# Optimization experiments

Measured on AMD Instinct MI355X. Metric: run time of the kernel, lower is better.

The kernel has to match this reference:

```python
import jax, jax.numpy as jnp
from jax import lax
import numpy as np

DIM = 192
WS = 8
HEADS = 6
HD = DIM // HEADS
SCALE = HD ** -0.5
EPS = 1e-6


def setup_inputs() -> dict:
    key = jax.random.key(0)
    ks = jax.random.split(key, 12)
    d = DIM
    inp = {
        "x": jax.random.normal(ks[0], (16, d, 128, 128), jnp.float32),
        "w_pre1": jax.random.normal(ks[1], (d, d), jnp.float32) * 0.02,
        "b_pre1": jnp.zeros((d,), jnp.float32),
        "w_dw": jax.random.normal(ks[2], (d, 1, 3, 3), jnp.float32) * 0.1,
        "b_dw": jnp.zeros((d,), jnp.float32),
        "ln_g": jnp.ones((d,), jnp.float32),
        "ln_b": jnp.zeros((d,), jnp.float32),
        "w_qkv": jax.random.normal(ks[3], (d, 3 * d), jnp.float32) * 0.02,
        "b_qkv": jnp.zeros((3 * d,), jnp.float32),
        "w1": jax.random.normal(ks[4], (d, 4 * d), jnp.float32) * 0.02,
        "b1": jnp.zeros((4 * d,), jnp.float32),
        "w2": jax.random.normal(ks[5], (4 * d, d), jnp.float32) * 0.02,
        "b2": jnp.zeros((d,), jnp.float32),
        "w_proj": jax.random.normal(ks[6], (d, d), jnp.float32) * 0.02,
        "b_proj": jnp.zeros((d,), jnp.float32),
    }
    return inp


def reference(x, w_pre1, b_pre1, w_dw, b_dw, ln_g, ln_b, w_qkv, b_qkv,
              w1, b1, w2, b2, w_proj, b_proj):
    B, C, H, W = x.shape
    shortcut = x
    # preprocess: 1x1 conv then 3x3 depthwise conv
    h = jnp.einsum('bchw,oc->bohw', x, w_pre1) + b_pre1[None, :, None, None]
    h = lax.conv_general_dilated(
        h, w_dw, window_strides=(1, 1), padding='SAME',
        feature_group_count=C,
        dimension_numbers=('NCHW', 'OIHW', 'NCHW')) + b_dw[None, :, None, None]
    # LayerNorm over channels (BHWC)
    h = h.transpose(0, 2, 3, 1)
    mu = h.mean(-1, keepdims=True)
    var = ((h - mu) ** 2).mean(-1, keepdims=True)
    h = (h - mu) / jnp.sqrt(var + EPS) * ln_g + ln_b
    # window partition (H, W divisible by WS -> no padding)
    nH, nW = H // WS, W // WS
    T = WS * WS
    p = h.reshape(B, nH, WS, nW, WS, C).transpose(0, 1, 3, 2, 4, 5)
    p = p.reshape(B * nH * nW, T, C)  # (N, T, C)
    N = p.shape[0]
    # QKV attention within each window
    qkv = (p @ w_qkv + b_qkv).reshape(N, T, 3, HEADS, HD)
    q = qkv[:, :, 0].transpose(0, 2, 1, 3)  # (N, h, T, hd)
    k = qkv[:, :, 1].transpose(0, 2, 1, 3)
    v = qkv[:, :, 2].transpose(0, 2, 1, 3)
    attn = jax.nn.softmax(jnp.einsum('nhtd,nhsd->nhts', q, k) * SCALE, axis=-1)
    out_attn = jnp.einsum('nhts,nhsd->nhtd', attn, v)
    out_attn = out_attn.transpose(0, 2, 1, 3).reshape(N, T, C)
    # gMLP branch
    out_gmlp = jax.nn.gelu(p @ w1 + b1, approximate=False) @ w2 + b2
    out = out_attn * out_gmlp
    # merge windows back to (B, C, H, W)
    out = out.reshape(B, nH, nW, WS, WS, C).transpose(0, 1, 3, 2, 4, 5)
    out = out.reshape(B, H, W, C).transpose(0, 3, 1, 2)
    out = jnp.einsum('bchw,oc->bohw', out, w_proj) + b_proj[None, :, None, None]
    return out + shortcut
```

## Files before the change

### kernel.cpp

```cpp
#include <hip/hip_runtime.h>
#include <hip/hip_bf16.h>
#include <math.h>


#define DIM    192
#define IMG_H  128
#define IMG_W  128
#define HW     16384
#define NB     16
#define NWIN   4096
#define NHEADS 6
#define HDIM   32
#define ATT_SCALE 0.17677669529663687f
#define LN_EPS 1e-6f

typedef __hip_bfloat16 bf16;
__device__ __forceinline__ float b2f(bf16 v) { return __bfloat162float(v); }
__device__ __forceinline__ bf16  f2b(float v) { return __float2bfloat16(v); }

typedef __bf16 bh8 __attribute__((ext_vector_type(8)));
typedef float  f32x4 __attribute__((ext_vector_type(4)));
#define MFMA16(a, b, c) __builtin_amdgcn_mfma_f32_16x16x32_bf16((a), (b), (c), 0, 0, 0)

__global__ __launch_bounds__(256) void k_prep(
    const float* __restrict__ src, bf16* __restrict__ dst, int K, int N)
{
    __shared__ float t[32][33];
    const int tid = threadIdx.x;
    const int lx = tid & 31, ly = tid >> 5;
    const int n0 = blockIdx.x * 32, k0 = blockIdx.y * 32;
    for (int r = ly; r < 32; r += 8)
        t[r][lx] = src[(size_t)(k0 + r) * N + n0 + lx];
    __syncthreads();
    for (int r = ly; r < 32; r += 8)
        dst[(size_t)(n0 + r) * K + k0 + lx] = f2b(t[lx][r]);
}

__global__ __launch_bounds__(256) void k_pre1(
    const float* __restrict__ x, const float* __restrict__ w,
    const float* __restrict__ bias, float* __restrict__ h1)
{
    __shared__ __align__(16) float lw[64 * 192];
    const int tid = threadIdx.x;
    const int obase = blockIdx.y * 64;
    for (int i = tid; i < 64 * 192; i += 256)
        lw[i] = w[obase * 192 + i];
    __syncthreads();

    const int g  = blockIdx.x * 256 + tid;
    const int b  = g >> 14;
    const int hw = g & (HW - 1);
    const float* xb = x + (size_t)b * DIM * HW + hw;

    float acc[64];
#pragma unroll
    for (int o = 0; o < 64; ++o) acc[o] = bias[obase + o];

    for (int c = 0; c < DIM; c += 4) {
        float xv0 = xb[(size_t)(c + 0) * HW];
        float xv1 = xb[(size_t)(c + 1) * HW];
        float xv2 = xb[(size_t)(c + 2) * HW];
        float xv3 = xb[(size_t)(c + 3) * HW];
#pragma unroll
        for (int o = 0; o < 64; ++o) {
            const float4 wv = *(const float4*)&lw[o * 192 + c];
            acc[o] += wv.x * xv0 + wv.y * xv1 + wv.z * xv2 + wv.w * xv3;
        }
    }
    float* hb = h1 + (size_t)b * DIM * HW + hw;
#pragma unroll
    for (int o = 0; o < 64; ++o) hb[(size_t)(obase + o) * HW] = acc[o];
}

__global__ __launch_bounds__(256) void k_dwln(
    const float* __restrict__ h1, const float* __restrict__ w_dw,
    const float* __restrict__ b_dw, const float* __restrict__ ln_g,
    const float* __restrict__ ln_b, bf16* __restrict__ p)
{
    __shared__ float tile[64 * 192];
    __shared__ float patch[32 * 101];
    const int tid = threadIdx.x;
    const int win = blockIdx.x;
    const int b = win >> 8, rem = win & 255;
    const int r0 = (rem >> 4) * 8, c0 = (rem & 15) * 8;

    for (int cc = 0; cc < 6; ++cc) {
        for (int i = tid; i < 3200; i += 256) {
            int ch = i / 100, pp = i % 100;
            int pr = pp / 10, pc = pp % 10;
            int gy = r0 - 1 + pr, gx = c0 - 1 + pc;
            float v = 0.f;
            if ((unsigned)gy < 128u && (unsigned)gx < 128u)
                v = h1[(((size_t)b * DIM + cc * 32 + ch) * IMG_H + gy) * IMG_W + gx];
            patch[ch * 101 + pp] = v;
        }
        __syncthreads();
        for (int i = tid; i < 2048; i += 256) {
            int pix = i >> 5, chl = i & 31;
            int ch = cc * 32 + chl;
            int r = pix >> 3, c = pix & 7;
            float acc = b_dw[ch];
#pragma unroll
            for (int ky = 0; ky < 3; ++ky)
#pragma unroll
                for (int kx = 0; kx < 3; ++kx)
                    acc = fmaf(w_dw[ch * 9 + ky * 3 + kx],
                               patch[chl * 101 + (r + ky) * 10 + (c + kx)], acc);
            tile[pix * 192 + ch] = acc;
        }
        __syncthreads();
    }
    const int pix = tid >> 2, sub = tid & 3;
    float s1 = 0.f, s2 = 0.f;
    for (int j = 0; j < 48; ++j) {
        float v = tile[pix * 192 + sub * 48 + j];
        s1 += v; s2 += v * v;
    }
    s1 += __shfl_xor(s1, 1); s2 += __shfl_xor(s2, 1);
    s1 += __shfl_xor(s1, 2); s2 += __shfl_xor(s2, 2);
    float mu  = s1 * (1.f / 192.f);
    float var = fmaxf(s2 * (1.f / 192.f) - mu * mu, 0.f);
    float rstd = rsqrtf(var + LN_EPS);
    bf16* pout = p + ((size_t)win * 64 + pix) * 192 + sub * 48;
    for (int j = 0; j < 48; ++j) {
        int c = sub * 48 + j;
        pout[j] = f2b((tile[pix * 192 + c] - mu) * rstd * ln_g[c] + ln_b[c]);
    }
}

__global__ __launch_bounds__(384) void k_attn(
    const bf16* __restrict__ p, const bf16* __restrict__ wqkvt,
    const float* __restrict__ b_qkv, bf16* __restrict__ a)
{
    __shared__ __align__(16) char smem[142848];
    bf16*  qs = (bf16*)(smem);
    bf16*  ks = (bf16*)(smem + 25600);
    bf16*  vT = (bf16*)(smem + 51200);
    bf16*  ps = (bf16*)(smem + 78848);
    bf16*  wt = (bf16*)(smem + 104448);
    bf16*  pbase = (bf16*)(smem + 78848);

    const int tid  = threadIdx.x;
    const int wave = tid >> 6, lane = tid & 63;
    const int lid  = lane & 15, lhi = lane >> 4;
    const int win  = blockIdx.x;
    const f32x4 zero4 = {0.f, 0.f, 0.f, 0.f};

    const bf16* pwin = p + (size_t)win * 64 * 192;
    for (int i = tid; i < 1536; i += 384) {
        int r = i / 24, c = (i % 24) * 8;
        *(bh8*)(ps + r * 200 + c) = *(const bh8*)(pwin + r * 192 + c);
    }

    const int mb  = (wave / 3) * 32;
    const int nbw = (wave % 3) * 32;
    for (int nc = 0; nc < 6; ++nc) {
        for (int i = tid; i < 2304; i += 384) {
            int r = i / 24, c = (i % 24) * 8;
            *(bh8*)(wt + r * 200 + c) =
                *(const bh8*)(wqkvt + (size_t)(nc * 96 + r) * 192 + c);
        }
        __syncthreads();

        f32x4 acc[2][2];
#pragma unroll
        for (int mi = 0; mi < 2; ++mi)
#pragma unroll
            for (int ni = 0; ni < 2; ++ni) {
                float b = b_qkv[nc * 96 + nbw + ni * 16 + lid];
                f32x4 bb = {b, b, b, b};
                acc[mi][ni] = bb;
            }
#pragma unroll
        for (int k8 = 0; k8 < 6; ++k8) {
            bh8 af[2], bfr[2];
#pragma unroll
            for (int mi = 0; mi < 2; ++mi)
                af[mi] = *(const bh8*)(ps + (mb + mi * 16 + lid) * 200 + k8 * 32 + 8 * lhi);
#pragma unroll
            for (int ni = 0; ni < 2; ++ni)
                bfr[ni] = *(const bh8*)(wt + (nbw + ni * 16 + lid) * 200 + k8 * 32 + 8 * lhi);
#pragma unroll
            for (int mi = 0; mi < 2; ++mi)
#pragma unroll
                for (int ni = 0; ni < 2; ++ni)
                    acc[mi][ni] = MFMA16(af[mi], bfr[ni], acc[mi][ni]);
        }
#pragma unroll
        for (int mi = 0; mi < 2; ++mi)
#pragma unroll
            for (int ni = 0; ni < 2; ++ni) {
                const int colg = nc * 96 + nbw + ni * 16 + lid;
#pragma unroll
                for (int r = 0; r < 4; ++r) {
                    const int t = mb + mi * 16 + 4 * lhi + r;
                    float v = acc[mi][ni][r];
                    if (colg < 192)       qs[t * 200 + colg] = f2b(v * ATT_SCALE);
                    else if (colg < 384)  ks[t * 200 + (colg - 192)] = f2b(v);
                    else                  vT[(colg - 384) * 72 + t] = f2b(v);
                }
            }
        __syncthreads();
    }

    const int h = wave;
    bf16* pw = pbase + wave * (64 * 72);

    f32x4 sacc[4][4];
    {
        bh8 qf[4], kf[4];
#pragma unroll
        for (int mi = 0; mi < 4; ++mi)
            qf[mi] = *(const bh8*)(qs + (mi * 16 + lid) * 200 + h * 32 + 8 * lhi);
#pragma unroll
        for (int ni = 0; ni < 4; ++ni)
            kf[ni] = *(const bh8*)(ks + (ni * 16 + lid) * 200 + h * 32 + 8 * lhi);
#pragma unroll
        for (int mi = 0; mi < 4; ++mi)
#pragma unroll
            for (int ni = 0; ni < 4; ++ni)
                sacc[mi][ni] = MFMA16(qf[mi], kf[ni], zero4);
    }

#pragma unroll
    for (int mi = 0; mi < 4; ++mi)
#pragma unroll
        for (int r = 0; r < 4; ++r) {
            float mx = fmaxf(fmaxf(sacc[mi][0][r], sacc[mi][1][r]),
                             fmaxf(sacc[mi][2][r], sacc[mi][3][r]));
            mx = fmaxf(mx, __shfl_xor(mx, 1));
            mx = fmaxf(mx, __shfl_xor(mx, 2));
            mx = fmaxf(mx, __shfl_xor(mx, 4));
            mx = fmaxf(mx, __shfl_xor(mx, 8));
            float e0 = __expf(sacc[mi][0][r] - mx);
            float e1 = __expf(sacc[mi][1][r] - mx);
            float e2 = __expf(sacc[mi][2][r] - mx);
            float e3 = __expf(sacc[mi][3][r] - mx);
            float sum = e0 + e1 + e2 + e3;
            sum += __shfl_xor(sum, 1);
            sum += __shfl_xor(sum, 2);
            sum += __shfl_xor(sum, 4);
            sum += __shfl_xor(sum, 8);
            float inv = 1.f / sum;
            sacc[mi][0][r] = e0 * inv;
            sacc[mi][1][r] = e1 * inv;
            sacc[mi][2][r] = e2 * inv;
            sacc[mi][3][r] = e3 * inv;
        }

#pragma unroll
    for (int mi = 0; mi < 4; ++mi)
#pragma unroll
        for (int ni = 0; ni < 4; ++ni)
#pragma unroll
            for (int r = 0; r < 4; ++r)
                pw[(mi * 16 + 4 * lhi + r) * 72 + ni * 16 + lid] = f2b(sacc[mi][ni][r]);
    asm volatile("s_waitcnt lgkmcnt(0)" ::: "memory");
    __builtin_amdgcn_sched_barrier(0);

    f32x4 oacc[4][2];
#pragma unroll
    for (int mi = 0; mi < 4; ++mi)
#pragma unroll
        for (int nb2 = 0; nb2 < 2; ++nb2) oacc[mi][nb2] = zero4;
#pragma unroll
    for (int kk = 0; kk < 2; ++kk) {
        bh8 pf[4];
#pragma unroll
        for (int mi = 0; mi < 4; ++mi)
            pf[mi] = *(const bh8*)(pw + (mi * 16 + lid) * 72 + kk * 32 + 8 * lhi);
#pragma unroll
        for (int nb2 = 0; nb2 < 2; ++nb2) {
            bh8 vf = *(const bh8*)(vT + (h * 32 + nb2 * 16 + lid) * 72 + kk * 32 + 8 * lhi);
#pragma unroll
            for (int mi = 0; mi < 4; ++mi)
                oacc[mi][nb2] = MFMA16(pf[mi], vf, oacc[mi][nb2]);
        }
    }
#pragma unroll
    for (int mi = 0; mi < 4; ++mi)
#pragma unroll
        for (int nb2 = 0; nb2 < 2; ++nb2)
#pragma unroll
            for (int r = 0; r < 4; ++r) {
                const int t = mi * 16 + 4 * lhi + r;
                a[((size_t)win * 64 + t) * 192 + h * 32 + nb2 * 16 + lid] =
                    f2b(oacc[mi][nb2][r]);
            }
}

__global__ __launch_bounds__(512) void k_gmlp(
    const bf16* __restrict__ p, const bf16* __restrict__ w1t,
    const float* __restrict__ b1, const bf16* __restrict__ w2t,
    const float* __restrict__ b2, bf16* __restrict__ a)
{
    __shared__ __align__(16) char smem[122880];
    bf16* ps  = (bf16*)(smem);
    bf16* w1c = (bf16*)(smem + 51200);
    bf16* w2c = (bf16*)(smem + 76800);
    bf16* hb  = (bf16*)(smem + 104448);

    const int tid  = threadIdx.x;
    const int wave = tid >> 6, lane = tid & 63;
    const int lid  = lane & 15, lhi = lane >> 4;
    const int win0 = blockIdx.x * 2;

    const bf16* pwin = p + (size_t)win0 * 64 * 192;
    for (int i = tid; i < 3072; i += 512) {
        int r = i / 24, c = (i % 24) * 8;
        *(bh8*)(ps + r * 200 + c) = *(const bh8*)(pwin + (size_t)r * 192 + c);
    }

    f32x4 acc2[12];
#pragma unroll
    for (int ni = 0; ni < 12; ++ni) {
        float b = b2[ni * 16 + lid];
        f32x4 bb = {b, b, b, b};
        acc2[ni] = bb;
    }
    const int mb = (wave >> 1) * 32, nb = (wave & 1) * 32;

    for (int hc = 0; hc < 12; ++hc) {
        for (int i = tid; i < 1536; i += 512) {
            int r = i / 24, c = (i % 24) * 8;
            *(bh8*)(w1c + r * 200 + c) =
                *(const bh8*)(w1t + (size_t)(hc * 64 + r) * 192 + c);
        }
        for (int i = tid; i < 1536; i += 512) {
            int r = i / 8, c = (i % 8) * 8;
            *(bh8*)(w2c + r * 72 + c) =
                *(const bh8*)(w2t + (size_t)r * 768 + hc * 64 + c);
        }
        __syncthreads();

        f32x4 acc1[2][2];
#pragma unroll
        for (int mi = 0; mi < 2; ++mi)
#pragma unroll
            for (int ni = 0; ni < 2; ++ni) {
                float b = b1[hc * 64 + nb + ni * 16 + lid];
                f32x4 bb = {b, b, b, b};
                acc1[mi][ni] = bb;
            }
#pragma unroll
        for (int k8 = 0; k8 < 6; ++k8) {
            bh8 af0 = *(const bh8*)(ps + (mb + lid) * 200 + k8 * 32 + 8 * lhi);
            bh8 af1 = *(const bh8*)(ps + (mb + 16 + lid) * 200 + k8 * 32 + 8 * lhi);
            bh8 bf0 = *(const bh8*)(w1c + (nb + lid) * 200 + k8 * 32 + 8 * lhi);
            bh8 bf1 = *(const bh8*)(w1c + (nb + 16 + lid) * 200 + k8 * 32 + 8 * lhi);
            acc1[0][0] = MFMA16(af0, bf0, acc1[0][0]);
            acc1[0][1] = MFMA16(af0, bf1, acc1[0][1]);
            acc1[1][0] = MFMA16(af1, bf0, acc1[1][0]);
            acc1[1][1] = MFMA16(af1, bf1, acc1[1][1]);
        }
#pragma unroll
        for (int mi = 0; mi < 2; ++mi)
#pragma unroll
            for (int ni = 0; ni < 2; ++ni)
#pragma unroll
                for (int r = 0; r < 4; ++r) {
                    int row = mb + mi * 16 + 4 * lhi + r;
                    int col = nb + ni * 16 + lid;
                    float xv = acc1[mi][ni][r];
                    hb[row * 72 + col] =
                        f2b(0.5f * xv * (1.f + erff(xv * 0.70710678118654752f)));
                }
        __syncthreads();

#pragma unroll
        for (int kk = 0; kk < 2; ++kk) {
            bh8 hf = *(const bh8*)(hb + (wave * 16 + lid) * 72 + kk * 32 + 8 * lhi);
#pragma unroll
            for (int ni = 0; ni < 12; ++ni) {
                bh8 wf = *(const bh8*)(w2c + (ni * 16 + lid) * 72 + kk * 32 + 8 * lhi);
                acc2[ni] = MFMA16(hf, wf, acc2[ni]);
            }
        }
        __syncthreads();
    }

    bf16* awin = a + (size_t)win0 * 64 * 192;
#pragma unroll
    for (int ni = 0; ni < 12; ++ni)
#pragma unroll
        for (int r = 0; r < 4; ++r) {
            int t = wave * 16 + 4 * lhi + r;
            int col = ni * 16 + lid;
            size_t idx = (size_t)t * 192 + col;
            awin[idx] = f2b(acc2[ni][r] * b2f(awin[idx]));
        }
}

__global__ __launch_bounds__(256) void k_proj(
    const bf16* __restrict__ m, const float* __restrict__ wp,
    const float* __restrict__ b_proj, const float* __restrict__ x,
    float* __restrict__ out)
{
    __shared__ __align__(16) char smem[128000];
    bf16*  mw = (bf16*)(smem);
    bf16*  wl = (bf16*)(smem + 51200);
    float* ot = (float*)(smem);

    const int tid  = threadIdx.x;
    const int wave = tid >> 6, lane = tid & 63;
    const int lid  = lane & 15, lhi = lane >> 4;
    const int bp   = blockIdx.x;
    const int b    = bp >> 7, rem = bp & 127;
    const int wr   = rem >> 3, wcp = rem & 7;
    const int win0 = b * 256 + wr * 16 + wcp * 2;
    const int r0   = wr * 8, c0 = wcp * 16;

    const bf16* msrc = m + (size_t)win0 * 64 * 192;
    for (int i = tid; i < 3072; i += 256) {
        int r = i / 24, c = (i % 24) * 8;
        *(bh8*)(mw + r * 200 + c) = *(const bh8*)(msrc + (size_t)r * 192 + c);
    }
    for (int i = tid; i < 9216; i += 256) {
        int r = i / 48, c = (i % 48) * 4;
        float4 v = *(const float4*)(wp + (size_t)r * 192 + c);
        bf16* d = wl + r * 200 + c;
        d[0] = f2b(v.x); d[1] = f2b(v.y); d[2] = f2b(v.z); d[3] = f2b(v.w);
    }
    __syncthreads();

    const int mb = wave * 32;
    f32x4 acc[2][12];
#pragma unroll
    for (int ni = 0; ni < 12; ++ni) {
        float bv = b_proj[ni * 16 + lid];
        f32x4 bb = {bv, bv, bv, bv};
        acc[0][ni] = bb;
        acc[1][ni] = bb;
    }
#pragma unroll
    for (int k8 = 0; k8 < 6; ++k8) {
        bh8 af0 = *(const bh8*)(mw + (mb + lid) * 200 + k8 * 32 + 8 * lhi);
        bh8 af1 = *(const bh8*)(mw + (mb + 16 + lid) * 200 + k8 * 32 + 8 * lhi);
#pragma unroll
        for (int ni = 0; ni < 12; ++ni) {
            bh8 bfr = *(const bh8*)(wl + (ni * 16 + lid) * 200 + k8 * 32 + 8 * lhi);
            acc[0][ni] = MFMA16(af0, bfr, acc[0][ni]);
            acc[1][ni] = MFMA16(af1, bfr, acc[1][ni]);
        }
    }
    __syncthreads();

#pragma unroll
    for (int mi = 0; mi < 2; ++mi)
#pragma unroll
        for (int ni = 0; ni < 12; ++ni)
#pragma unroll
            for (int r = 0; r < 4; ++r)
                ot[(mb + mi * 16 + 4 * lhi + r) * 193 + ni * 16 + lid] = acc[mi][ni][r];
    __syncthreads();

    for (int i = tid; i < 24576; i += 256) {
        int o = i >> 7, pix = i & 127;
        int r = pix >> 4, cc = pix & 15;
        int trow = ((cc >> 3) << 6) + r * 8 + (cc & 7);
        size_t idx = (((size_t)b * DIM + o) * IMG_H + r0 + r) * IMG_W + c0 + cc;
        out[idx] = ot[trow * 193 + o] + x[idx];
    }
}

extern "C" void kernel_launch(void* const* d_in, const int* in_sizes, int n_in,
                              void* d_out, int out_size, void* d_ws, size_t ws_size,
                              hipStream_t stream)
{
    const float* x      = (const float*)d_in[0];
    const float* w_pre1 = (const float*)d_in[1];
    const float* b_pre1 = (const float*)d_in[2];
    const float* w_dw   = (const float*)d_in[3];
    const float* b_dw   = (const float*)d_in[4];
    const float* ln_g   = (const float*)d_in[5];
    const float* ln_b   = (const float*)d_in[6];
    const float* w_qkv  = (const float*)d_in[7];
    const float* b_qkv  = (const float*)d_in[8];
    const float* w1     = (const float*)d_in[9];
    const float* b1     = (const float*)d_in[10];
    const float* w2     = (const float*)d_in[11];
    const float* b2     = (const float*)d_in[12];
    const float* w_proj = (const float*)d_in[13];
    const float* b_proj = (const float*)d_in[14];
    float* out = (float*)d_out;

    const size_t NELEM = (size_t)NB * DIM * HW;
    float* h1 = (float*)d_out;
    bf16* p = (bf16*)d_ws;
    bf16* a = p + NELEM;
    bf16* wqkvt = a + NELEM;
    bf16* w1t   = wqkvt + 3 * DIM * DIM;
    bf16* w2t   = w1t + 4 * DIM * DIM;

    k_prep<<<dim3(18, 6),  256, 0, stream>>>(w_qkv, wqkvt, DIM, 3 * DIM);
    k_prep<<<dim3(24, 6),  256, 0, stream>>>(w1, w1t, DIM, 4 * DIM);
    k_prep<<<dim3(6, 24),  256, 0, stream>>>(w2, w2t, 4 * DIM, DIM);

    k_pre1<<<dim3(1024, 3), 256, 0, stream>>>(x, w_pre1, b_pre1, h1);
    k_dwln<<<dim3(NWIN), 256, 0, stream>>>(h1, w_dw, b_dw, ln_g, ln_b, p);
    k_attn<<<dim3(NWIN), 384, 0, stream>>>(p, wqkvt, b_qkv, a);
    k_gmlp<<<dim3(NWIN / 2), 512, 0, stream>>>(p, w1t, b1, w2t, b2, a);
    k_proj<<<dim3(NWIN / 2), 256, 0, stream>>>(a, w_proj, b_proj, x, out);
}
```

Before: 2.158 ms.

## Move pre-conv 1x1 projection to bf16 MFMA with transposed input staging

Adds a transpose kernel that converts x from NCHW fp32 into pixel-major bf16, reusing the p workspace. The 1x1 pre-projection is rewritten as an MFMA 16x16x32 bf16 GEMM over 128-pixel tiles against all 192 output channels. The result is staged through LDS and written back in NCHW. This replaces a scalar fp32 FMA loop with matrix-core math, at the cost of an extra transpose pass over x, bf16 rounding of x and weights, and 128KB of LDS per block, which limits occupancy. The weights are converted to bf16 again in every block.

New measurement: 1.963 ms. 9.0% less time.

```diff
diff --git a/kernel.cpp b/kernel.cpp
--- a/kernel.cpp
+++ b/kernel.cpp
@@ -36,40 +36,87 @@
         dst[(size_t)(n0 + r) * K + k0 + lx] = f2b(t[lx][r]);
 }
 
+__global__ __launch_bounds__(256) void k_xpose(
+    const float* __restrict__ x, bf16* __restrict__ xt)
+{
+    __shared__ float t[32][33];
+    const int tid = threadIdx.x;
+    const int lx = tid & 31, ly = tid >> 5;
+    const int n0 = blockIdx.x * 32;
+    const int k0 = blockIdx.y * 32;
+    const float* src = x + (size_t)blockIdx.z * DIM * HW;
+    bf16* dst = xt + (size_t)blockIdx.z * HW * DIM;
+    for (int r = ly; r < 32; r += 8)
+        t[r][lx] = src[(size_t)(k0 + r) * HW + n0 + lx];
+    __syncthreads();
+    for (int r = ly; r < 32; r += 8)
+        dst[(size_t)(n0 + r) * DIM + k0 + lx] = f2b(t[lx][r]);
+}
+
 __global__ __launch_bounds__(256) void k_pre1(
-    const float* __restrict__ x, const float* __restrict__ w,
+    const bf16* __restrict__ xt, const float* __restrict__ wp,
     const float* __restrict__ bias, float* __restrict__ h1)
 {
-    __shared__ __align__(16) float lw[64 * 192];
-    const int tid = threadIdx.x;
-    const int obase = blockIdx.y * 64;
-    for (int i = tid; i < 64 * 192; i += 256)
-        lw[i] = w[obase * 192 + i];
-    __syncthreads();
-
-    const int g  = blockIdx.x * 256 + tid;
-    const int b  = g >> 14;
-    const int hw = g & (HW - 1);
-    const float* xb = x + (size_t)b * DIM * HW + hw;
-
-    float acc[64];
-#pragma unroll
-    for (int o = 0; o < 64; ++o) acc[o] = bias[obase + o];
-
-    for (int c = 0; c < DIM; c += 4) {
-        float xv0 = xb[(size_t)(c + 0) * HW];
-        float xv1 = xb[(size_t)(c + 1) * HW];
-        float xv2 = xb[(size_t)(c + 2) * HW];
-        float xv3 = xb[(size_t)(c + 3) * HW];
-#pragma unroll
-        for (int o = 0; o < 64; ++o) {
-            const float4 wv = *(const float4*)&lw[o * 192 + c];
-            acc[o] += wv.x * xv0 + wv.y * xv1 + wv.z * xv2 + wv.w * xv3;
-        }
-    }
-    float* hb = h1 + (size_t)b * DIM * HW + hw;
-#pragma unroll
-    for (int o = 0; o < 64; ++o) hb[(size_t)(obase + o) * HW] = acc[o];
+    __shared__ __align__(16) char smem[128000];
+    bf16*  mw = (bf16*)(smem);
+    bf16*  wl = (bf16*)(smem + 51200);
+    float* ot = (float*)(smem);
+
+    const int tid  = threadIdx.x;
+    const int wave = tid >> 6, lane = tid & 63;
+    const int lid  = lane & 15, lhi = lane >> 4;
+    const int g0   = blockIdx.x * 128;
+    const int b    = g0 >> 14;
+    const int hw0  = g0 & (HW - 1);
+
+    const bf16* msrc = xt + (size_t)g0 * DIM;
+    for (int i = tid; i < 3072; i += 256) {
+        int r = i / 24, c = (i % 24) * 8;
+        *(bh8*)(mw + r * 200 + c) = *(const bh8*)(msrc + (size_t)r * 192 + c);
+    }
+    for (int i = tid; i < 9216; i += 256) {
+        int r = i / 48, c = (i % 48) * 4;
+        float4 v = *(const float4*)(wp + (size_t)r * 192 + c);
+        bf16* d = wl + r * 200 + c;
+        d[0] = f2b(v.x); d[1] = f2b(v.y); d[2] = f2b(v.z); d[3] = f2b(v.w);
+    }
+    __syncthreads();
+
+    const int mb = wave * 32;
+    f32x4 acc[2][12];
+#pragma unroll
+    for (int ni = 0; ni < 12; ++ni) {
+        float bv = bias[ni * 16 + lid];
+        f32x4 bb = {bv, bv, bv, bv};
+        acc[0][ni] = bb;
+        acc[1][ni] = bb;
+    }
+#pragma unroll
+    for (int k8 = 0; k8 < 6; ++k8) {
+        bh8 af0 = *(const bh8*)(mw + (mb + lid) * 200 + k8 * 32 + 8 * lhi);
+        bh8 af1 = *(const bh8*)(mw + (mb + 16 + lid) * 200 + k8 * 32 + 8 * lhi);
+#pragma unroll
+        for (int ni = 0; ni < 12; ++ni) {
+            bh8 bfr = *(const bh8*)(wl + (ni * 16 + lid) * 200 + k8 * 32 + 8 * lhi);
+            acc[0][ni] = MFMA16(af0, bfr, acc[0][ni]);
+            acc[1][ni] = MFMA16(af1, bfr, acc[1][ni]);
+        }
+    }
+    __syncthreads();
+
+#pragma unroll
+    for (int mi = 0; mi < 2; ++mi)
+#pragma unroll
+        for (int ni = 0; ni < 12; ++ni)
+#pragma unroll
+            for (int r = 0; r < 4; ++r)
+                ot[(mb + mi * 16 + 4 * lhi + r) * 193 + ni * 16 + lid] = acc[mi][ni][r];
+    __syncthreads();
+
+    for (int i = tid; i < 24576; i += 256) {
+        int o = i >> 7, pix = i & 127;
+        h1[((size_t)b * DIM + o) * HW + hw0 + pix] = ot[pix * 193 + o];
+    }
 }
 
 __global__ __launch_bounds__(256) void k_dwln(
@@ -496,7 +543,9 @@
     k_prep<<<dim3(24, 6),  256, 0, stream>>>(w1, w1t, DIM, 4 * DIM);
     k_prep<<<dim3(6, 24),  256, 0, stream>>>(w2, w2t, 4 * DIM, DIM);
 
-    k_pre1<<<dim3(1024, 3), 256, 0, stream>>>(x, w_pre1, b_pre1, h1);
+    bf16* xt = p;
+    k_xpose<<<dim3(HW / 32, DIM / 32, NB), 256, 0, stream>>>(x, xt);
+    k_pre1<<<dim3(2048), 256, 0, stream>>>(xt, w_pre1, b_pre1, h1);
     k_dwln<<<dim3(NWIN), 256, 0, stream>>>(h1, w_dw, b_dw, ln_g, ln_b, p);
     k_attn<<<dim3(NWIN), 384, 0, stream>>>(p, wqkvt, b_qkv, a);
     k_gmlp<<<dim3(NWIN / 2), 512, 0, stream>>>(p, w1t, b1, w2t, b2, a);
```
